# Performance work log

Measured on AMD Instinct MI355X. Metric: run time of the kernel, lower is better.

Reference implementation:

```python
import jax, jax.numpy as jnp
import numpy as np

N = 100000      # nodes
E = 1600000     # edges
G = 1024        # graphs in batch
NF = 9          # atom features (OGB AtomEncoder)
V = 128         # vocab per atom feature
H = 128         # hidden_dim
L = 3           # num_graph_layers
OUT = 10        # output_dim
BN_EPS = 1e-5


def setup_inputs() -> dict:
    key = jax.random.key(0)
    ks = jax.random.split(key, 12)
    x = jax.random.randint(ks[0], (N, NF), 0, V, dtype=jnp.int32)
    edge_index = jax.random.randint(ks[1], (2, E), 0, N, dtype=jnp.int32)
    batch = jnp.sort(jax.random.randint(ks[2], (N,), 0, G, dtype=jnp.int32))
    emb = jax.random.normal(ks[3], (NF, V, H), dtype=jnp.float32) * 0.05
    Ws = jax.random.normal(ks[4], (L, H, H), dtype=jnp.float32) * (1.0 / np.sqrt(H))
    bs = jnp.zeros((L, H), dtype=jnp.float32)
    gamma = jnp.ones((L - 1, H), dtype=jnp.float32)
    beta = jnp.zeros((L - 1, H), dtype=jnp.float32)
    run_mean = jax.random.normal(ks[5], (L - 1, H), dtype=jnp.float32) * 0.1
    run_var = jax.random.uniform(ks[6], (L - 1, H), minval=0.5, maxval=1.5, dtype=jnp.float32)
    W_clf = jax.random.normal(ks[7], (H, OUT), dtype=jnp.float32) * (1.0 / np.sqrt(H))
    b_clf = jnp.zeros((OUT,), dtype=jnp.float32)
    return {"x": x, "edge_index": edge_index, "batch": batch, "emb": emb,
            "Ws": Ws, "bs": bs, "gamma": gamma, "beta": beta,
            "run_mean": run_mean, "run_var": run_var,
            "W_clf": W_clf, "b_clf": b_clf}


def reference(x, edge_index, batch, emb, Ws, bs, gamma, beta, run_mean, run_var, W_clf, b_clf):
    # Eval-mode forward: dropout = identity, BatchNorm uses running stats.
    src, dst = edge_index[0], edge_index[1]
    # GCN symmetric normalization with self-loops: deg = 1 + in-degree
    deg = jax.ops.segment_sum(jnp.ones((E,), jnp.float32), dst, num_segments=N) + 1.0
    dinv = jax.lax.rsqrt(deg)                 # [N]
    norm_e = dinv[src] * dinv[dst]            # [E] edge coefficient
    norm_self = dinv * dinv                   # [N] self-loop coefficient

    # AtomEncoder: sum of per-feature embedding lookups -> [N, H]
    h = emb[jnp.arange(NF)[None, :], x].sum(axis=1)

    for i in range(L):
        hw = h @ Ws[i]                                                       # [N, H]
        h = (jax.ops.segment_sum(hw[src] * norm_e[:, None], dst, num_segments=N)
             + hw * norm_self[:, None] + bs[i])                              # GCNConv
        if i < L - 1:
            h = (h - run_mean[i]) * (gamma[i] * jax.lax.rsqrt(run_var[i] + BN_EPS)) + beta[i]
            h = jax.nn.relu(h)

    # global mean pool over graphs
    counts = jax.ops.segment_sum(jnp.ones((N,), jnp.float32), batch, num_segments=G)
    pooled = jax.ops.segment_sum(h, batch, num_segments=G) / jnp.maximum(counts, 1.0)[:, None]
    return pooled @ W_clf + b_clf             # [G, OUT]
```

## Files before the change

### kernel.cpp

```cpp
#include <hip/hip_runtime.h>
#include <hip/hip_bf16.h>
#include <hip/hip_fp16.h>

#define NN 100000
#define EE 1600000
#define GG 1024
#define NF 9
#define VV 128
#define HH 128
#define LL 3
#define OUTD 10
#define BN_EPS 1e-5f
#define NB_SCAN 98
#define NBUCK 196
#define BCAP 12288
#define CHUNK 4096

typedef __attribute__((ext_vector_type(8))) short short8;
typedef __attribute__((ext_vector_type(4))) float f32x4;

__device__ inline unsigned short f2bf(float x) {
    unsigned u = __float_as_uint(x);
    unsigned r = (u + 0x7fffu + ((u >> 16) & 1u)) >> 16;
    return (unsigned short)r;
}
__device__ inline float bf2f(unsigned short b) { return __uint_as_float(((unsigned)b) << 16); }

__device__ inline void mix8(float a[8], const uint4& r, float nm) {
    asm("v_fma_mix_f32 %0, %8, %12, %0 op_sel:[0,0,0] op_sel_hi:[1,0,0]\n\t"
        "v_fma_mix_f32 %1, %8, %12, %1 op_sel:[1,0,0] op_sel_hi:[1,0,0]\n\t"
        "v_fma_mix_f32 %2, %9, %12, %2 op_sel:[0,0,0] op_sel_hi:[1,0,0]\n\t"
        "v_fma_mix_f32 %3, %9, %12, %3 op_sel:[1,0,0] op_sel_hi:[1,0,0]\n\t"
        "v_fma_mix_f32 %4, %10, %12, %4 op_sel:[0,0,0] op_sel_hi:[1,0,0]\n\t"
        "v_fma_mix_f32 %5, %10, %12, %5 op_sel:[1,0,0] op_sel_hi:[1,0,0]\n\t"
        "v_fma_mix_f32 %6, %11, %12, %6 op_sel:[0,0,0] op_sel_hi:[1,0,0]\n\t"
        "v_fma_mix_f32 %7, %11, %12, %7 op_sel:[1,0,0] op_sel_hi:[1,0,0]"
        : "+v"(a[0]), "+v"(a[1]), "+v"(a[2]), "+v"(a[3]),
          "+v"(a[4]), "+v"(a[5]), "+v"(a[6]), "+v"(a[7])
        : "v"(r.x), "v"(r.y), "v"(r.z), "v"(r.w), "v"(nm));
}

__global__ __launch_bounds__(256) void split_kernel(const int* __restrict__ src,
                                                    const int* __restrict__ dst,
                                                    int* __restrict__ bcur,
                                                    int* __restrict__ bucket_edges) {
    __shared__ int lcnt[256], loff[256], lcur[256], gbase[256], sh[256];
    __shared__ int stage[CHUNK];
    __shared__ unsigned char stageb[CHUNK];
    int tid = threadIdx.x;
    int cs = blockIdx.x * CHUNK;
    int n = min(CHUNK, EE - cs);
    lcnt[tid] = 0;
    __syncthreads();
    for (int i = tid; i < n; i += 256)
        atomicAdd(&lcnt[dst[cs + i] >> 9], 1);
    __syncthreads();
    int val = lcnt[tid];
    sh[tid] = val; __syncthreads();
    for (int d = 1; d < 256; d <<= 1) {
        int t = (tid >= d) ? sh[tid - d] : 0;
        __syncthreads();
        sh[tid] += t;
        __syncthreads();
    }
    loff[tid] = sh[tid] - val;
    lcur[tid] = sh[tid] - val;
    __syncthreads();
    for (int i = tid; i < n; i += 256) {
        int d = dst[cs + i], s = src[cs + i];
        int b = d >> 9;
        int p = atomicAdd(&lcur[b], 1);
        stage[p] = (s << 9) | (d & 511);
        stageb[p] = (unsigned char)b;
    }
    if (val > 0) gbase[tid] = atomicAdd(&bcur[tid], val);
    __syncthreads();
    for (int i = tid; i < n; i += 256) {
        int b = stageb[i];
        bucket_edges[(size_t)b * BCAP + gbase[b] + (i - loff[b])] = stage[i];
    }
}

__global__ __launch_bounds__(256) void bhist_kernel(const int* __restrict__ bcur,
                                                    const int* __restrict__ bucket_edges,
                                                    int* __restrict__ cnt) {
    __shared__ int lc[512];
    int b = blockIdx.x, tid = threadIdx.x;
    lc[tid] = 0; lc[tid + 256] = 0;
    __syncthreads();
    int n = bcur[b];
    const int* be = bucket_edges + (size_t)b * BCAP;
    for (int i = tid; i < n; i += 256) atomicAdd(&lc[be[i] & 511], 1);
    __syncthreads();
    int node = b * 512 + tid;
    if (node < NN) cnt[node] = lc[tid];
    node += 256;
    if (node < NN) cnt[node] = lc[tid + 256];
}

__global__ void scanA_kernel(const int* __restrict__ cnt, int* __restrict__ bsum,
                             float* __restrict__ dinv) {
    __shared__ int sh[256];
    int tid = threadIdx.x;
    int base = blockIdx.x * 1024 + tid * 4;
    int s = 0;
#pragma unroll
    for (int i = 0; i < 4; ++i) {
        int idx = base + i;
        if (idx < NN) {
            int c = cnt[idx];
            s += c;
            dinv[idx] = rsqrtf(1.0f + (float)c);
        }
    }
    sh[tid] = s; __syncthreads();
    for (int d = 128; d > 0; d >>= 1) { if (tid < d) sh[tid] += sh[tid + d]; __syncthreads(); }
    if (tid == 0) bsum[blockIdx.x] = sh[0];
}

__global__ void scanB_kernel(int* __restrict__ bsum) {
    __shared__ int sh[128];
    int tid = threadIdx.x;
    int v = (tid < NB_SCAN) ? bsum[tid] : 0;
    sh[tid] = v; __syncthreads();
    for (int d = 1; d < 128; d <<= 1) {
        int t = (tid >= d) ? sh[tid - d] : 0;
        __syncthreads();
        sh[tid] += t;
        __syncthreads();
    }
    if (tid < NB_SCAN) bsum[tid] = sh[tid] - v;
}

__global__ void scanC_kernel(const int* __restrict__ cnt, const int* __restrict__ bsum,
                             int* __restrict__ row_ptr) {
    __shared__ int sh[256];
    int tid = threadIdx.x;
    int base = blockIdx.x * 1024 + tid * 4;
    int v[4];
#pragma unroll
    for (int i = 0; i < 4; ++i) { int idx = base + i; v[i] = (idx < NN) ? cnt[idx] : 0; }
    int tsum = v[0] + v[1] + v[2] + v[3];
    sh[tid] = tsum; __syncthreads();
    for (int d = 1; d < 256; d <<= 1) {
        int t = (tid >= d) ? sh[tid - d] : 0;
        __syncthreads();
        sh[tid] += t;
        __syncthreads();
    }
    int excl = sh[tid] - tsum + bsum[blockIdx.x];
#pragma unroll
    for (int i = 0; i < 4; ++i) {
        int idx = base + i;
        if (idx < NN) row_ptr[idx] = excl;
        excl += v[i];
    }
    if (blockIdx.x == 0 && tid == 0) row_ptr[NN] = EE;
}

__global__ __launch_bounds__(256) void cscatter_kernel(const int* __restrict__ bcur,
                                                       const int* __restrict__ bucket_edges,
                                                       const int* __restrict__ row_ptr,
                                                       const float* __restrict__ dinv,
                                                       int2* __restrict__ col) {
    __shared__ int lcur[512];
    int b = blockIdx.x, tid = threadIdx.x;
    int node0 = b * 512;
#pragma unroll
    for (int k = 0; k < 2; ++k) {
        int j = tid + k * 256;
        int node = node0 + j;
        if (node < NN) lcur[j] = row_ptr[node];
    }
    __syncthreads();
    int n = bcur[b];
    const int* be = bucket_edges + (size_t)b * BCAP;
    for (int i = tid; i < n; i += 256) {
        int w = be[i];
        int j = w & 511;
        int s = (int)((unsigned)w >> 9);
        int p = atomicAdd(&lcur[j], 1);
        float nm = dinv[s] * dinv[node0 + j];
        col[p] = make_int2(s, __float_as_int(nm));
    }
}

__global__ void wconv_kernel(const float* __restrict__ Ws,
                             unsigned short* __restrict__ WThi,
                             unsigned short* __restrict__ WTlo) {
    int id = blockIdx.x * 256 + threadIdx.x;
    if (id >= LL * HH * HH) return;
    int layer = id >> 14;
    int rem = id & (HH * HH - 1);
    int k = rem >> 7, n = rem & 127;
    float w = Ws[id];
    unsigned short hi = f2bf(w);
    float lo = w - bf2f(hi);
    WThi[(size_t)layer * HH * HH + n * HH + k] = hi;
    WTlo[(size_t)layer * HH * HH + n * HH + k] = f2bf(lo);
}

__global__ __launch_bounds__(256) void enc_mm_kernel(const int* __restrict__ x,
        const float* __restrict__ emb,
        const unsigned short* __restrict__ WThi, const unsigned short* __restrict__ WTlo,
        __half* __restrict__ hw_out) {
    __shared__ __align__(16) unsigned short lh[32][136];
    __shared__ __align__(16) unsigned short ll[32][136];
    int tid = threadIdx.x;
    int nloc = tid >> 3;
    int seg = tid & 7;
    int nodebase = blockIdx.x * 32;
    int n = nodebase + nloc;
    float s[16];
#pragma unroll
    for (int i = 0; i < 16; ++i) s[i] = 0.f;
#pragma unroll
    for (int f = 0; f < NF; ++f) {
        int idx = x[n * NF + f];
        const float4* ep = (const float4*)(emb + ((size_t)(f * VV + idx)) * HH + seg * 16);
#pragma unroll
        for (int q = 0; q < 4; ++q) {
            float4 e = ep[q];
            s[q * 4 + 0] += e.x; s[q * 4 + 1] += e.y;
            s[q * 4 + 2] += e.z; s[q * 4 + 3] += e.w;
        }
    }
#pragma unroll
    for (int q = 0; q < 4; ++q) {
        ushort4 oh, ol;
        oh.x = f2bf(s[q * 4 + 0]); ol.x = f2bf(s[q * 4 + 0] - bf2f(oh.x));
        oh.y = f2bf(s[q * 4 + 1]); ol.y = f2bf(s[q * 4 + 1] - bf2f(oh.y));
        oh.z = f2bf(s[q * 4 + 2]); ol.z = f2bf(s[q * 4 + 2] - bf2f(oh.z));
        oh.w = f2bf(s[q * 4 + 3]); ol.w = f2bf(s[q * 4 + 3] - bf2f(oh.w));
        *(ushort4*)&lh[nloc][seg * 16 + q * 4] = oh;
        *(ushort4*)&ll[nloc][seg * 16 + q * 4] = ol;
    }
    __syncthreads();
    int wave = tid >> 6, lane = tid & 63;
    int quad = lane >> 4, m = lane & 15;
    f32x4 acc[2][2] = {};
    int kq = quad * 8;
#pragma unroll
    for (int t = 0; t < 4; ++t) {
        int k0 = t * 32 + kq;
        short8 a0h = *(const short8*)&lh[m][k0];
        short8 a0l = *(const short8*)&ll[m][k0];
        short8 a1h = *(const short8*)&lh[16 + m][k0];
        short8 a1l = *(const short8*)&ll[16 + m][k0];
#pragma unroll
        for (int c = 0; c < 2; ++c) {
            int ct = wave * 2 + c;
            short8 bh = *(const short8*)(WThi + (size_t)(ct * 16 + m) * HH + k0);
            short8 bl = *(const short8*)(WTlo + (size_t)(ct * 16 + m) * HH + k0);
            acc[0][c] = __builtin_amdgcn_mfma_f32_16x16x32_bf16(a0h, bh, acc[0][c], 0, 0, 0);
            acc[0][c] = __builtin_amdgcn_mfma_f32_16x16x32_bf16(a0l, bh, acc[0][c], 0, 0, 0);
            acc[0][c] = __builtin_amdgcn_mfma_f32_16x16x32_bf16(a0h, bl, acc[0][c], 0, 0, 0);
            acc[1][c] = __builtin_amdgcn_mfma_f32_16x16x32_bf16(a1h, bh, acc[1][c], 0, 0, 0);
            acc[1][c] = __builtin_amdgcn_mfma_f32_16x16x32_bf16(a1l, bh, acc[1][c], 0, 0, 0);
            acc[1][c] = __builtin_amdgcn_mfma_f32_16x16x32_bf16(a1h, bl, acc[1][c], 0, 0, 0);
        }
    }
#pragma unroll
    for (int c = 0; c < 2; ++c) {
        int colx = (wave * 2 + c) * 16 + m;
#pragma unroll
        for (int rt = 0; rt < 2; ++rt) {
            int r0 = nodebase + rt * 16 + quad * 4;
#pragma unroll
            for (int reg = 0; reg < 4; ++reg)
                hw_out[(size_t)(r0 + reg) * HH + colx] = __float2half(acc[rt][c][reg]);
        }
    }
}

__device__ inline void gather_node(const uint4* __restrict__ hw4,
                                   const int2* __restrict__ col,
                                   int start, int end, int c4,
                                   float a[8], float b[8]) {
    int e = start;
    for (; e + 4 <= end; e += 4) {
        unsigned long long w0 = *(const unsigned long long*)&col[e];
        unsigned long long w1 = *(const unsigned long long*)&col[e + 1];
        unsigned long long w2 = *(const unsigned long long*)&col[e + 2];
        unsigned long long w3 = *(const unsigned long long*)&col[e + 3];
        uint4 r0 = hw4[(size_t)(unsigned)(w0 & 0xffffffffu) * 16 + c4];
        uint4 r1 = hw4[(size_t)(unsigned)(w1 & 0xffffffffu) * 16 + c4];
        uint4 r2 = hw4[(size_t)(unsigned)(w2 & 0xffffffffu) * 16 + c4];
        uint4 r3 = hw4[(size_t)(unsigned)(w3 & 0xffffffffu) * 16 + c4];
        mix8(a, r0, __int_as_float((int)(unsigned)(w0 >> 32)));
        mix8(b, r1, __int_as_float((int)(unsigned)(w1 >> 32)));
        mix8(a, r2, __int_as_float((int)(unsigned)(w2 >> 32)));
        mix8(b, r3, __int_as_float((int)(unsigned)(w3 >> 32)));
    }
    if (e < end) {
        int last = end - 1;
        int e1 = min(e + 1, last), e2 = min(e + 2, last), e3 = min(e + 3, last);
        unsigned long long w0 = *(const unsigned long long*)&col[e];
        unsigned long long w1 = *(const unsigned long long*)&col[e1];
        unsigned long long w2 = *(const unsigned long long*)&col[e2];
        unsigned long long w3 = *(const unsigned long long*)&col[e3];
        float n0 = __int_as_float((int)(unsigned)(w0 >> 32));
        float n1 = (e + 1 < end) ? __int_as_float((int)(unsigned)(w1 >> 32)) : 0.f;
        float n2 = (e + 2 < end) ? __int_as_float((int)(unsigned)(w2 >> 32)) : 0.f;
        float n3 = (e + 3 < end) ? __int_as_float((int)(unsigned)(w3 >> 32)) : 0.f;
        uint4 r0 = hw4[(size_t)(unsigned)(w0 & 0xffffffffu) * 16 + c4];
        uint4 r1 = hw4[(size_t)(unsigned)(w1 & 0xffffffffu) * 16 + c4];
        uint4 r2 = hw4[(size_t)(unsigned)(w2 & 0xffffffffu) * 16 + c4];
        uint4 r3 = hw4[(size_t)(unsigned)(w3 & 0xffffffffu) * 16 + c4];
        mix8(a, r0, n0);
        mix8(b, r1, n1);
        mix8(a, r2, n2);
        mix8(b, r3, n3);
    }
}

__global__ __launch_bounds__(512) void agg_mm_kernel(const __half* __restrict__ hw_in,
    const int* __restrict__ row_ptr, const int2* __restrict__ col,
    const float* __restrict__ dinv,
    const float* __restrict__ bias, const float* __restrict__ gamma,
    const float* __restrict__ beta, const float* __restrict__ rmean,
    const float* __restrict__ rvar,
    const unsigned short* __restrict__ WThi, const unsigned short* __restrict__ WTlo,
    __half* __restrict__ hw_out) {
    __shared__ __align__(16) unsigned short lh[32][136];
    __shared__ __align__(16) unsigned short ll[32][136];
    int wave = threadIdx.x >> 6;
    int lane = threadIdx.x & 63;
    int grp = lane >> 4;
    int c4 = lane & 15;
    int nodebase = blockIdx.x * 32;
    const uint4* hw4 = (const uint4*)hw_in;

    int v = nodebase + wave * 4 + grp;
    int start = row_ptr[v], end = row_ptr[v + 1];
    float a[8] = {}, b[8] = {};
    gather_node(hw4, col, start, end, c4, a, b);

    {
        float dv = dinv[v];
        uint4 r = hw4[(size_t)v * 16 + c4];
        mix8(a, r, dv * dv);
    }
#pragma unroll
    for (int i = 0; i < 8; ++i) a[i] += b[i];

    int ch = c4 * 8;
#pragma unroll
    for (int i = 0; i < 8; ++i) a[i] += bias[ch + i];
#pragma unroll
    for (int i = 0; i < 8; ++i) {
        int c = ch + i;
        float sc = gamma[c] * rsqrtf(rvar[c] + BN_EPS);
        a[i] = fmaxf((a[i] - rmean[c]) * sc + beta[c], 0.f);
    }
    int rloc = wave * 4 + grp;
    ushort4 oh0, oh1, ol0, ol1;
    oh0.x = f2bf(a[0]); ol0.x = f2bf(a[0] - bf2f(oh0.x));
    oh0.y = f2bf(a[1]); ol0.y = f2bf(a[1] - bf2f(oh0.y));
    oh0.z = f2bf(a[2]); ol0.z = f2bf(a[2] - bf2f(oh0.z));
    oh0.w = f2bf(a[3]); ol0.w = f2bf(a[3] - bf2f(oh0.w));
    oh1.x = f2bf(a[4]); ol1.x = f2bf(a[4] - bf2f(oh1.x));
    oh1.y = f2bf(a[5]); ol1.y = f2bf(a[5] - bf2f(oh1.y));
    oh1.z = f2bf(a[6]); ol1.z = f2bf(a[6] - bf2f(oh1.z));
    oh1.w = f2bf(a[7]); ol1.w = f2bf(a[7] - bf2f(oh1.w));
    *(ushort4*)&lh[rloc][ch]     = oh0;
    *(ushort4*)&lh[rloc][ch + 4] = oh1;
    *(ushort4*)&ll[rloc][ch]     = ol0;
    *(ushort4*)&ll[rloc][ch + 4] = ol1;

    __syncthreads();
    int quad = lane >> 4, m = lane & 15;
    f32x4 acc[2] = {};
    int kq = quad * 8;
    int ct = wave;
#pragma unroll
    for (int t = 0; t < 4; ++t) {
        int k0 = t * 32 + kq;
        short8 a0h = *(const short8*)&lh[m][k0];
        short8 a0l = *(const short8*)&ll[m][k0];
        short8 a1h = *(const short8*)&lh[16 + m][k0];
        short8 a1l = *(const short8*)&ll[16 + m][k0];
        short8 bh = *(const short8*)(WThi + (size_t)(ct * 16 + m) * HH + k0);
        short8 bl = *(const short8*)(WTlo + (size_t)(ct * 16 + m) * HH + k0);
        acc[0] = __builtin_amdgcn_mfma_f32_16x16x32_bf16(a0h, bh, acc[0], 0, 0, 0);
        acc[0] = __builtin_amdgcn_mfma_f32_16x16x32_bf16(a0l, bh, acc[0], 0, 0, 0);
        acc[0] = __builtin_amdgcn_mfma_f32_16x16x32_bf16(a0h, bl, acc[0], 0, 0, 0);
        acc[1] = __builtin_amdgcn_mfma_f32_16x16x32_bf16(a1h, bh, acc[1], 0, 0, 0);
        acc[1] = __builtin_amdgcn_mfma_f32_16x16x32_bf16(a1l, bh, acc[1], 0, 0, 0);
        acc[1] = __builtin_amdgcn_mfma_f32_16x16x32_bf16(a1h, bl, acc[1], 0, 0, 0);
    }
    int colx = ct * 16 + m;
#pragma unroll
    for (int rt = 0; rt < 2; ++rt) {
        int r0 = nodebase + rt * 16 + quad * 4;
#pragma unroll
        for (int reg = 0; reg < 4; ++reg)
            hw_out[(size_t)(r0 + reg) * HH + colx] = __float2half(acc[rt][reg]);
    }
}

__global__ __launch_bounds__(512) void agg_pool_kernel(const __half* __restrict__ hw_in,
    const int* __restrict__ row_ptr, const int2* __restrict__ col,
    const float* __restrict__ dinv, const float* __restrict__ bias,
    const int* __restrict__ batch, float* __restrict__ pooled) {
    __shared__ __align__(16) float lf[32][132];
    __shared__ int bg[32];
    int wave = threadIdx.x >> 6;
    int lane = threadIdx.x & 63;
    int grp = lane >> 4;
    int c4 = lane & 15;
    int nodebase = blockIdx.x * 32;
    const uint4* hw4 = (const uint4*)hw_in;

    int v = nodebase + wave * 4 + grp;
    int start = row_ptr[v], end = row_ptr[v + 1];
    float a[8] = {}, b[8] = {};
    gather_node(hw4, col, start, end, c4, a, b);

    {
        float dv = dinv[v];
        uint4 r = hw4[(size_t)v * 16 + c4];
        mix8(a, r, dv * dv);
    }
#pragma unroll
    for (int i = 0; i < 8; ++i) a[i] += b[i];

    int ch = c4 * 8;
    int rloc = wave * 4 + grp;
#pragma unroll
    for (int i = 0; i < 8; ++i) lf[rloc][ch + i] = a[i] + bias[ch + i];
    if (c4 == 0) bg[rloc] = batch[v];

    __syncthreads();
    int c = threadIdx.x & 127;
    int rh = threadIdx.x >> 7;
    int r0 = rh * 8;
    int curg = bg[r0];
    float run = 0.f;
    for (int r = r0; r < r0 + 8; ++r) {
        int gg = bg[r];
        if (gg != curg) {
            atomicAdd(&pooled[(size_t)curg * HH + c], run);
            run = 0.f; curg = gg;
        }
        run += lf[r][c];
    }
    atomicAdd(&pooled[(size_t)curg * HH + c], run);
}

__global__ __launch_bounds__(128) void clf_kernel(const float* __restrict__ pooled,
    const int* __restrict__ batch, const float* __restrict__ Wc,
    const float* __restrict__ bc, float* __restrict__ out) {
    __shared__ float pl[HH];
    int g = blockIdx.x;
    int tid = threadIdx.x;
    int lo = 0, hi = NN;
    while (lo < hi) { int mid = (lo + hi) >> 1; if (batch[mid] < g) lo = mid + 1; else hi = mid; }
    int start = lo;
    lo = 0; hi = NN;
    int g1 = g + 1;
    while (lo < hi) { int mid = (lo + hi) >> 1; if (batch[mid] < g1) lo = mid + 1; else hi = mid; }
    float cnt = (float)(lo - start);
    pl[tid] = pooled[(size_t)g * HH + tid] / fmaxf(cnt, 1.0f);
    __syncthreads();
    if (tid < OUTD) {
        float acc = bc[tid];
#pragma unroll 16
        for (int c = 0; c < HH; ++c) acc += pl[c] * Wc[c * OUTD + tid];
        out[g * OUTD + tid] = acc;
    }
}

extern "C" void kernel_launch(void* const* d_in, const int* in_sizes, int n_in,
                              void* d_out, int out_size, void* d_ws, size_t ws_size,
                              hipStream_t stream) {
    const int*   x      = (const int*)d_in[0];
    const int*   eidx   = (const int*)d_in[1];
    const int*   batch  = (const int*)d_in[2];
    const float* emb    = (const float*)d_in[3];
    const float* Ws     = (const float*)d_in[4];
    const float* bs     = (const float*)d_in[5];
    const float* gamma  = (const float*)d_in[6];
    const float* beta   = (const float*)d_in[7];
    const float* rmean  = (const float*)d_in[8];
    const float* rvar   = (const float*)d_in[9];
    const float* Wclf   = (const float*)d_in[10];
    const float* bclf   = (const float*)d_in[11];
    float* out = (float*)d_out;

    const int* e_src = eidx;
    const int* e_dst = eidx + EE;

    char* ws = (char*)d_ws;
    size_t off = 0;
    auto take = [&](size_t bytes) -> void* {
        void* p = ws + off;
        off = (off + bytes + 255) & ~(size_t)255;
        return p;
    };
    float* dinv     = (float*)take((size_t)NN * 4);
    int*   cnt      = (int*)  take((size_t)NN * 4);
    int*   row_ptr  = (int*)  take((size_t)(NN + 1) * 4);
    int*   bsum     = (int*)  take((size_t)NB_SCAN * 4);
    int*   bcur     = (int*)  take((size_t)256 * 4);
    int*   bucket_edges = (int*)take((size_t)NBUCK * BCAP * 4);
    int2*  col      = (int2*) take((size_t)EE * 8);
    __half* hwA     = (__half*)take((size_t)NN * HH * 2);
    __half* hwB     = (__half*)take((size_t)NN * HH * 2);
    float* pooled   = (float*)take((size_t)GG * HH * 4);
    unsigned short* WThi = (unsigned short*)take((size_t)LL * HH * HH * 2);
    unsigned short* WTlo = (unsigned short*)take((size_t)LL * HH * HH * 2);

    hipMemsetAsync(bcur, 0, 256 * 4, stream);
    hipMemsetAsync(pooled, 0, (size_t)GG * HH * 4, stream);

    split_kernel<<<(EE + CHUNK - 1) / CHUNK, 256, 0, stream>>>(e_src, e_dst, bcur, bucket_edges);
    bhist_kernel<<<NBUCK, 256, 0, stream>>>(bcur, bucket_edges, cnt);
    scanA_kernel<<<NB_SCAN, 256, 0, stream>>>(cnt, bsum, dinv);
    scanB_kernel<<<1, 128, 0, stream>>>(bsum);
    scanC_kernel<<<NB_SCAN, 256, 0, stream>>>(cnt, bsum, row_ptr);
    cscatter_kernel<<<NBUCK, 256, 0, stream>>>(bcur, bucket_edges, row_ptr, dinv, col);
    wconv_kernel<<<(LL * HH * HH + 255) / 256, 256, 0, stream>>>(Ws, WThi, WTlo);

    enc_mm_kernel<<<NN / 32, 256, 0, stream>>>(x, emb, WThi, WTlo, hwA);
    agg_mm_kernel<<<NN / 32, 512, 0, stream>>>(hwA, row_ptr, col, dinv,
        bs, gamma, beta, rmean, rvar,
        WThi + (size_t)1 * HH * HH, WTlo + (size_t)1 * HH * HH, hwB);
    agg_mm_kernel<<<NN / 32, 512, 0, stream>>>(hwB, row_ptr, col, dinv,
        bs + HH, gamma + HH, beta + HH, rmean + HH, rvar + HH,
        WThi + (size_t)2 * HH * HH, WTlo + (size_t)2 * HH * HH, hwA);
    agg_pool_kernel<<<NN / 32, 512, 0, stream>>>(hwA, row_ptr, col, dinv,
        bs + 2 * HH, batch, pooled);

    clf_kernel<<<GG, 128, 0, stream>>>(pooled, batch, Wclf, bclf, out);
}
```

Baseline: 424.9 us.

## Project last layer to classifier width before aggregation and pooling

Uses linearity to apply the classifier weights to the final-layer node features before the sparse aggregation and mean pool, so the edge gather runs on 16 padded fp32 channels instead of 128 half channels. A new MFMA projection kernel computes per-node 10-wide outputs with split fp16 hi/lo weights, and the layer bias is folded through the classifier as a precomputed vector. Pooling and the final kernel now work on 16-wide rows. This adds an extra kernel pass and some rounding change from the fp16 projection in exchange for much less gather traffic in the last aggregation.

```diff
diff --git a/kernel.cpp b/kernel.cpp
--- a/kernel.cpp
+++ b/kernel.cpp
@@ -15,8 +15,10 @@
 #define NBUCK 196
 #define BCAP 12288
 #define CHUNK 4096
+#define NB64 1563
 
 typedef __attribute__((ext_vector_type(8))) short short8;
+typedef __attribute__((ext_vector_type(8))) _Float16 half8;
 typedef __attribute__((ext_vector_type(4))) float f32x4;
 
 __device__ inline unsigned short f2bf(float x) {
@@ -38,6 +40,11 @@
         : "+v"(a[0]), "+v"(a[1]), "+v"(a[2]), "+v"(a[3]),
           "+v"(a[4]), "+v"(a[5]), "+v"(a[6]), "+v"(a[7])
         : "v"(r.x), "v"(r.y), "v"(r.z), "v"(r.w), "v"(nm));
+}
+
+__device__ inline void fma4(float4& a, const float4 r, float nm) {
+    a.x = fmaf(r.x, nm, a.x); a.y = fmaf(r.y, nm, a.y);
+    a.z = fmaf(r.z, nm, a.z); a.w = fmaf(r.w, nm, a.w);
 }
 
 __global__ __launch_bounds__(256) void split_kernel(const int* __restrict__ src,
@@ -198,6 +205,26 @@
     float lo = w - bf2f(hi);
     WThi[(size_t)layer * HH * HH + n * HH + k] = hi;
     WTlo[(size_t)layer * HH * HH + n * HH + k] = f2bf(lo);
+}
+
+__global__ __launch_bounds__(256) void prep_clf_kernel(const float* __restrict__ Wc,
+        const float* __restrict__ b2,
+        _Float16* __restrict__ WcThi, _Float16* __restrict__ WcTlo,
+        float* __restrict__ bb2) {
+    int tid = threadIdx.x;
+    for (int id = tid; id < 16 * HH; id += 256) {
+        int n = id >> 7, k = id & 127;
+        float w = (n < OUTD) ? Wc[k * OUTD + n] : 0.f;
+        _Float16 hi = (_Float16)w;
+        float lo = w - (float)hi;
+        WcThi[id] = hi;
+        WcTlo[id] = (_Float16)lo;
+    }
+    if (tid < OUTD) {
+        float s = 0.f;
+        for (int c = 0; c < HH; ++c) s += b2[c] * Wc[c * OUTD + tid];
+        bb2[tid] = s;
+    }
 }
 
 __global__ __launch_bounds__(256) void enc_mm_kernel(const int* __restrict__ x,
@@ -399,76 +426,123 @@
     }
 }
 
-__global__ __launch_bounds__(512) void agg_pool_kernel(const __half* __restrict__ hw_in,
+__global__ __launch_bounds__(256) void yproj_kernel(const __half* __restrict__ hw_in,
+        const _Float16* __restrict__ WcThi, const _Float16* __restrict__ WcTlo,
+        float* __restrict__ y) {
+    int tid = threadIdx.x;
+    int wv = tid >> 6, lane = tid & 63;
+    int quad = lane >> 4, m = lane & 15;
+    int nodebase = blockIdx.x * 64 + wv * 16;
+    int an = min(nodebase + m, NN - 1);
+    f32x4 acc = {};
+#pragma unroll
+    for (int t = 0; t < 4; ++t) {
+        int k0 = t * 32 + quad * 8;
+        half8 a  = *(const half8*)(hw_in + (size_t)an * HH + k0);
+        half8 bh = *(const half8*)(WcThi + m * HH + k0);
+        half8 bl = *(const half8*)(WcTlo + m * HH + k0);
+        acc = __builtin_amdgcn_mfma_f32_16x16x32_f16(a, bh, acc, 0, 0, 0);
+        acc = __builtin_amdgcn_mfma_f32_16x16x32_f16(a, bl, acc, 0, 0, 0);
+    }
+#pragma unroll
+    for (int reg = 0; reg < 4; ++reg) {
+        int node = nodebase + quad * 4 + reg;
+        if (node < NN) y[(size_t)node * 16 + m] = acc[reg];
+    }
+}
+
+__global__ __launch_bounds__(256) void agg_pool10_kernel(const float* __restrict__ y,
     const int* __restrict__ row_ptr, const int2* __restrict__ col,
-    const float* __restrict__ dinv, const float* __restrict__ bias,
-    const int* __restrict__ batch, float* __restrict__ pooled) {
-    __shared__ __align__(16) float lf[32][132];
-    __shared__ int bg[32];
-    int wave = threadIdx.x >> 6;
-    int lane = threadIdx.x & 63;
-    int grp = lane >> 4;
-    int c4 = lane & 15;
-    int nodebase = blockIdx.x * 32;
-    const uint4* hw4 = (const uint4*)hw_in;
-
-    int v = nodebase + wave * 4 + grp;
-    int start = row_ptr[v], end = row_ptr[v + 1];
-    float a[8] = {}, b[8] = {};
-    gather_node(hw4, col, start, end, c4, a, b);
-
-    {
+    const float* __restrict__ dinv, const int* __restrict__ batch,
+    float* __restrict__ pooled) {
+    __shared__ __align__(16) float lz[64][16];
+    __shared__ int bg[64];
+    int tid = threadIdx.x;
+    int g4 = tid >> 2;
+    int c = tid & 3;
+    int nodebase = blockIdx.x * 64;
+    int v = nodebase + g4;
+    int vc = min(v, NN - 1);
+    int start = row_ptr[vc];
+    int end = (v < NN) ? row_ptr[vc + 1] : start;
+    const float4* y4 = (const float4*)y;
+    float4 a = {0.f, 0.f, 0.f, 0.f}, b = {0.f, 0.f, 0.f, 0.f};
+    int e = start;
+    for (; e + 4 <= end; e += 4) {
+        unsigned long long w0 = *(const unsigned long long*)&col[e];
+        unsigned long long w1 = *(const unsigned long long*)&col[e + 1];
+        unsigned long long w2 = *(const unsigned long long*)&col[e + 2];
+        unsigned long long w3 = *(const unsigned long long*)&col[e + 3];
+        float4 r0 = y4[(size_t)(unsigned)(w0 & 0xffffffffu) * 4 + c];
+        float4 r1 = y4[(size_t)(unsigned)(w1 & 0xffffffffu) * 4 + c];
+        float4 r2 = y4[(size_t)(unsigned)(w2 & 0xffffffffu) * 4 + c];
+        float4 r3 = y4[(size_t)(unsigned)(w3 & 0xffffffffu) * 4 + c];
+        fma4(a, r0, __int_as_float((int)(unsigned)(w0 >> 32)));
+        fma4(b, r1, __int_as_float((int)(unsigned)(w1 >> 32)));
+        fma4(a, r2, __int_as_float((int)(unsigned)(w2 >> 32)));
+        fma4(b, r3, __int_as_float((int)(unsigned)(w3 >> 32)));
+    }
+    if (e < end) {
+        int last = end - 1;
+        int e1 = min(e + 1, last), e2 = min(e + 2, last), e3 = min(e + 3, last);
+        unsigned long long w0 = *(const unsigned long long*)&col[e];
+        unsigned long long w1 = *(const unsigned long long*)&col[e1];
+        unsigned long long w2 = *(const unsigned long long*)&col[e2];
+        unsigned long long w3 = *(const unsigned long long*)&col[e3];
+        float n0 = __int_as_float((int)(unsigned)(w0 >> 32));
+        float n1 = (e + 1 < end) ? __int_as_float((int)(unsigned)(w1 >> 32)) : 0.f;
+        float n2 = (e + 2 < end) ? __int_as_float((int)(unsigned)(w2 >> 32)) : 0.f;
+        float n3 = (e + 3 < end) ? __int_as_float((int)(unsigned)(w3 >> 32)) : 0.f;
+        float4 r0 = y4[(size_t)(unsigned)(w0 & 0xffffffffu) * 4 + c];
+        float4 r1 = y4[(size_t)(unsigned)(w1 & 0xffffffffu) * 4 + c];
+        float4 r2 = y4[(size_t)(unsigned)(w2 & 0xffffffffu) * 4 + c];
+        float4 r3 = y4[(size_t)(unsigned)(w3 & 0xffffffffu) * 4 + c];
+        fma4(a, r0, n0);
+        fma4(b, r1, n1);
+        fma4(a, r2, n2);
+        fma4(b, r3, n3);
+    }
+    if (v < NN) {
         float dv = dinv[v];
-        uint4 r = hw4[(size_t)v * 16 + c4];
-        mix8(a, r, dv * dv);
-    }
-#pragma unroll
-    for (int i = 0; i < 8; ++i) a[i] += b[i];
-
-    int ch = c4 * 8;
-    int rloc = wave * 4 + grp;
-#pragma unroll
-    for (int i = 0; i < 8; ++i) lf[rloc][ch + i] = a[i] + bias[ch + i];
-    if (c4 == 0) bg[rloc] = batch[v];
-
-    __syncthreads();
-    int c = threadIdx.x & 127;
-    int rh = threadIdx.x >> 7;
-    int r0 = rh * 8;
-    int curg = bg[r0];
+        float4 r = y4[(size_t)v * 4 + c];
+        fma4(a, r, dv * dv);
+    }
+    a.x += b.x; a.y += b.y; a.z += b.z; a.w += b.w;
+    *(float4*)&lz[g4][c * 4] = a;
+    if (c == 0) bg[g4] = batch[vc];
+    __syncthreads();
+    int ch = tid & 15;
+    int rh = tid >> 4;
+    int r0i = rh * 4;
+    int curg = bg[r0i];
     float run = 0.f;
-    for (int r = r0; r < r0 + 8; ++r) {
+    for (int r = r0i; r < r0i + 4; ++r) {
         int gg = bg[r];
         if (gg != curg) {
-            atomicAdd(&pooled[(size_t)curg * HH + c], run);
+            atomicAdd(&pooled[(size_t)curg * 16 + ch], run);
             run = 0.f; curg = gg;
         }
-        run += lf[r][c];
-    }
-    atomicAdd(&pooled[(size_t)curg * HH + c], run);
-}
-
-__global__ __launch_bounds__(128) void clf_kernel(const float* __restrict__ pooled,
-    const int* __restrict__ batch, const float* __restrict__ Wc,
+        run += lz[r][ch];
+    }
+    atomicAdd(&pooled[(size_t)curg * 16 + ch], run);
+}
+
+__global__ __launch_bounds__(256) void finalize_kernel(const float* __restrict__ pooled,
+    const int* __restrict__ batch, const float* __restrict__ bb2,
     const float* __restrict__ bc, float* __restrict__ out) {
-    __shared__ float pl[HH];
-    int g = blockIdx.x;
-    int tid = threadIdx.x;
+    int id = blockIdx.x * 256 + threadIdx.x;
+    if (id >= GG * 16) return;
+    int g = id >> 4, o = id & 15;
+    if (o >= OUTD) return;
     int lo = 0, hi = NN;
     while (lo < hi) { int mid = (lo + hi) >> 1; if (batch[mid] < g) lo = mid + 1; else hi = mid; }
-    int start = lo;
+    int s0 = lo;
     lo = 0; hi = NN;
     int g1 = g + 1;
     while (lo < hi) { int mid = (lo + hi) >> 1; if (batch[mid] < g1) lo = mid + 1; else hi = mid; }
-    float cnt = (float)(lo - start);
-    pl[tid] = pooled[(size_t)g * HH + tid] / fmaxf(cnt, 1.0f);
-    __syncthreads();
-    if (tid < OUTD) {
-        float acc = bc[tid];
-#pragma unroll 16
-        for (int c = 0; c < HH; ++c) acc += pl[c] * Wc[c * OUTD + tid];
-        out[g * OUTD + tid] = acc;
-    }
+    int cnt = lo - s0;
+    float r = pooled[(size_t)g * 16 + o] / fmaxf((float)cnt, 1.0f);
+    out[(size_t)g * OUTD + o] = r + ((cnt > 0) ? bb2[o] : 0.f) + bc[o];
 }
 
 extern "C" void kernel_launch(void* const* d_in, const int* in_sizes, int n_in,
@@ -507,12 +581,16 @@
     int2*  col      = (int2*) take((size_t)EE * 8);
     __half* hwA     = (__half*)take((size_t)NN * HH * 2);
     __half* hwB     = (__half*)take((size_t)NN * HH * 2);
-    float* pooled   = (float*)take((size_t)GG * HH * 4);
+    float* y        = (float*)take((size_t)NN * 16 * 4);
+    float* pooled   = (float*)take((size_t)GG * 16 * 4);
     unsigned short* WThi = (unsigned short*)take((size_t)LL * HH * HH * 2);
     unsigned short* WTlo = (unsigned short*)take((size_t)LL * HH * HH * 2);
+    _Float16* WcThi = (_Float16*)take((size_t)16 * HH * 2);
+    _Float16* WcTlo = (_Float16*)take((size_t)16 * HH * 2);
+    float* bb2      = (float*)take((size_t)16 * 4);
 
     hipMemsetAsync(bcur, 0, 256 * 4, stream);
-    hipMemsetAsync(pooled, 0, (size_t)GG * HH * 4, stream);
+    hipMemsetAsync(pooled, 0, (size_t)GG * 16 * 4, stream);
 
     split_kernel<<<(EE + CHUNK - 1) / CHUNK, 256, 0, stream>>>(e_src, e_dst, bcur, bucket_edges);
     bhist_kernel<<<NBUCK, 256, 0, stream>>>(bcur, bucket_edges, cnt);
@@ -521,6 +599,7 @@
     scanC_kernel<<<NB_SCAN, 256, 0, stream>>>(cnt, bsum, row_ptr);
     cscatter_kernel<<<NBUCK, 256, 0, stream>>>(bcur, bucket_edges, row_ptr, dinv, col);
     wconv_kernel<<<(LL * HH * HH + 255) / 256, 256, 0, stream>>>(Ws, WThi, WTlo);
+    prep_clf_kernel<<<1, 256, 0, stream>>>(Wclf, bs + 2 * HH, WcThi, WcTlo, bb2);
 
     enc_mm_kernel<<<NN / 32, 256, 0, stream>>>(x, emb, WThi, WTlo, hwA);
     agg_mm_kernel<<<NN / 32, 512, 0, stream>>>(hwA, row_ptr, col, dinv,
@@ -529,8 +608,7 @@
     agg_mm_kernel<<<NN / 32, 512, 0, stream>>>(hwB, row_ptr, col, dinv,
         bs + HH, gamma + HH, beta + HH, rmean + HH, rvar + HH,
         WThi + (size_t)2 * HH * HH, WTlo + (size_t)2 * HH * HH, hwA);
-    agg_pool_kernel<<<NN / 32, 512, 0, stream>>>(hwA, row_ptr, col, dinv,
-        bs + 2 * HH, batch, pooled);
-
-    clf_kernel<<<GG, 128, 0, stream>>>(pooled, batch, Wclf, bclf, out);
-}
+    yproj_kernel<<<NB64, 256, 0, stream>>>(hwA, WcThi, WcTlo, y);
+    agg_pool10_kernel<<<NB64, 256, 0, stream>>>(y, row_ptr, col, dinv, batch, pooled);
+    finalize_kernel<<<(GG * 16 + 255) / 256, 256, 0, stream>>>(pooled, batch, bb2, bclf, out);
+}
```

Result: faster. 412.0 us (-3.0%).
